# Optimization experiments

Measured on AMD Instinct MI355X. Metric: run time of the kernel, lower is better.

The kernel has to match this reference:

```python
import jax, jax.numpy as jnp
import numpy as np

N = 20000      # nodes
E = 160000     # edges (avg degree 8)
DIM_IN = 6     # node_dim_in (3 pos + 3 extra)
DIM = 3        # spatial dim used for edge vectors
L = 128        # node_dim_latent
A = 8          # atom_type_embed_dim
NL = 4         # nlayers
NMAX = 20      # nmax_atom_types
MAX_R = 50.0   # max_radius
EIN = 2 * L + 2 * A + 1  # message MLP input: y_src, y_dst, edge_attr(2A+1)


def smooth_cutoff(x):
    # e3nn-style smooth cutoff: 1 for x<0.5, cos ramp on [0.5,1], 0 beyond
    u = 2.0 * (x - 1.0)
    y = 0.5 * (1.0 - jnp.cos(jnp.pi * u))
    y = jnp.where(u > 0.0, 0.0, y)
    y = jnp.where(u < -1.0, 1.0, y)
    return y


def setup_inputs() -> dict:
    key = jax.random.key(0)
    ks = jax.random.split(key, 14)
    x = jax.random.normal(ks[0], (N, DIM_IN), dtype=jnp.float32) * 2.0
    batch = jnp.zeros((N,), dtype=jnp.int32)  # single graph; unused (con_fnc=None)
    node_attr = jax.random.randint(ks[1], (N, 1), 0, NMAX, dtype=jnp.int32)
    edge_src = jax.random.randint(ks[2], (E,), 0, N, dtype=jnp.int32)
    off = jax.random.randint(ks[3], (E,), 1, N, dtype=jnp.int32)
    edge_dst = (edge_src + off) % N  # no self-loops -> edge_len > 0
    # orthogonal uplift/project weight (torch parametrizations.orthogonal)
    W, _ = jnp.linalg.qr(jax.random.normal(ks[4], (L, DIM_IN), dtype=jnp.float32))  # [L, DIM_IN], orthonormal cols
    embed = jax.random.normal(ks[5], (NMAX, A), dtype=jnp.float32)
    h = jnp.ones((NL,), dtype=jnp.float32) * 0.01
    msg_w1 = jax.random.normal(ks[6], (NL, EIN, L), dtype=jnp.float32) / np.sqrt(EIN)
    msg_b1 = jnp.zeros((NL, L), dtype=jnp.float32)
    msg_w2 = jax.random.normal(ks[7], (NL, L, L), dtype=jnp.float32) / np.sqrt(L)
    msg_b2 = jnp.zeros((NL, L), dtype=jnp.float32)
    node_w1 = jax.random.normal(ks[8], (NL, 2 * L, L), dtype=jnp.float32) / np.sqrt(2 * L)
    node_b1 = jnp.zeros((NL, L), dtype=jnp.float32)
    node_w2 = jax.random.normal(ks[9], (NL, L, L), dtype=jnp.float32) / np.sqrt(L)
    node_b2 = jnp.zeros((NL, L), dtype=jnp.float32)
    return {"x": x, "batch": batch, "node_attr": node_attr, "edge_src": edge_src,
            "edge_dst": edge_dst, "W": W, "embed": embed, "h": h,
            "msg_w1": msg_w1, "msg_b1": msg_b1, "msg_w2": msg_w2, "msg_b2": msg_b2,
            "node_w1": node_w1, "node_b1": node_b1, "node_w2": node_w2, "node_b2": node_b2}


def _block(y, edge_attr, edge_src, edge_dst, w1, b1, w2, b2, nw1, nb1, nw2, nb2):
    # gather-compute-scatter message passing block
    m_in = jnp.concatenate([y[edge_src], y[edge_dst], edge_attr], axis=-1)  # [E, EIN]
    m = jax.nn.silu(m_in @ w1 + b1) @ w2 + b2                                # [E, L]
    agg = jax.ops.segment_sum(m, edge_dst, num_segments=N)                   # [N, L]
    u = jnp.concatenate([y, agg], axis=-1)                                   # [N, 2L]
    return jax.nn.silu(u @ nw1 + nb1) @ nw2 + nb2                            # [N, L]


def reference(x, batch, node_attr, edge_src, edge_dst, W, embed, h,
              msg_w1, msg_b1, msg_w2, msg_b2, node_w1, node_b1, node_w2, node_b2):
    attr_e = embed[jnp.min(node_attr, axis=-1)]  # [N, A]
    y = x @ W.T                                   # uplift [N, L]
    y_old = y
    for i in range(NL):
        pos = x[:, :DIM]
        edge_vec = pos[edge_src] - pos[edge_dst]
        edge_len = jnp.linalg.norm(edge_vec, axis=1)
        w = smooth_cutoff(edge_len / MAX_R) / edge_len
        edge_attr = jnp.concatenate([attr_e[edge_src], attr_e[edge_dst], w[:, None]], axis=-1)
        y_new = _block(y, edge_attr, edge_src, edge_dst,
                       msg_w1[i], msg_b1[i], msg_w2[i], msg_b2[i],
                       node_w1[i], node_b1[i], node_w2[i], node_b2[i])
        # leapfrog (gamma = 0)
        tmp = y
        y = 2.0 * y - y_old - (h[i] ** 2) * y_new
        y_old = tmp
        x = y @ W  # project back to low dim
    cv = jnp.float32(-1.0)
    reg = jnp.float32(0.0)
    return (x, cv, cv, reg, reg)
```

## Files before the change

### kernel.cpp

```cpp
#include <hip/hip_runtime.h>
#include <hip/hip_bf16.h>
#include <math.h>

#define N_ 20000
#define NPAD_ 20032
#define E_ 160000
#define DIM_IN_ 6
#define L_ 128
#define A_ 8
#define NL_ 4
#define EIN_ 273
#define MAX_R_ 50.0f

typedef unsigned short u16;
typedef short bf16x8 __attribute__((ext_vector_type(8)));
typedef u16   u16x8  __attribute__((ext_vector_type(8)));
typedef float f32x4  __attribute__((ext_vector_type(4)));

static __device__ __forceinline__ float bf2f(u16 u) {
    return __uint_as_float(((unsigned)u) << 16);
}
static __device__ __forceinline__ u16 f2bf(float f) {
    unsigned b = __float_as_uint(f);
    return (u16)((b + 0x7FFF + ((b >> 16) & 1)) >> 16);
}
static __device__ __forceinline__ float silu(float v) {
    return v / (1.f + __expf(-v));
}


__global__ void k_init_y(const float* __restrict__ x, const float* __restrict__ W,
                         float* __restrict__ y, float* __restrict__ y_old) {
    int tid = blockIdx.x * blockDim.x + threadIdx.x;
    if (tid >= N_ * L_) return;
    int n = tid >> 7, l = tid & 127;
    float a = 0.f;
#pragma unroll
    for (int d = 0; d < DIM_IN_; ++d) a = fmaf(x[n * DIM_IN_ + d], W[l * DIM_IN_ + d], a);
    y[tid] = a;
    y_old[tid] = a;
}

__global__ void k_attr(const int* __restrict__ node_attr, const float* __restrict__ embed,
                       float* __restrict__ attr_e) {
    int tid = blockIdx.x * blockDim.x + threadIdx.x;
    if (tid >= N_ * A_) return;
    int n = tid >> 3, a = tid & 7;
    attr_e[tid] = embed[node_attr[n] * A_ + a];
}

__global__ void k_pos(const float* __restrict__ y, const float* __restrict__ W,
                      const float* __restrict__ x_in, int layer,
                      float* __restrict__ pos4) {
    int tid = blockIdx.x * blockDim.x + threadIdx.x;
    if (tid >= N_ * 4) return;
    int n = tid >> 2, d = tid & 3;
    float v = 0.f;
    if (d < 3) {
        if (layer == 0) v = x_in[n * DIM_IN_ + d];
        else {
            for (int l = 0; l < L_; ++l) v = fmaf(y[(size_t)n * L_ + l], W[l * DIM_IN_ + d], v);
        }
    }
    pos4[tid] = v;
}

__global__ void k_x(const float* __restrict__ y, const float* __restrict__ W,
                    float* __restrict__ x_out) {
    int tid = blockIdx.x * blockDim.x + threadIdx.x;
    if (tid >= N_ * DIM_IN_) return;
    int n = tid / DIM_IN_, d = tid % DIM_IN_;
    float a = 0.f;
    for (int l = 0; l < L_; ++l) a = fmaf(y[(size_t)n * L_ + l], W[l * DIM_IN_ + d], a);
    x_out[tid] = a;
}

__global__ void k_scalars(float* __restrict__ tail) {
    int j = threadIdx.x;
    if (j < 4) tail[j] = (j < 2) ? -1.0f : 0.0f;
}


__global__ void k_hist(const int* __restrict__ edst, int* __restrict__ deg) {
    int e = blockIdx.x * blockDim.x + threadIdx.x;
    if (e < E_) atomicAdd(&deg[edst[e]], 1);
}

#define SCAN_CH 20
__global__ __launch_bounds__(1024) void k_scan(const int* __restrict__ deg,
                                               int* __restrict__ rowptr,
                                               int* __restrict__ cursor) {
    __shared__ int s[1024];
    int t = threadIdx.x;
    int base = t * SCAN_CH;
    int local[SCAN_CH];
    int sum = 0;
#pragma unroll
    for (int j = 0; j < SCAN_CH; ++j) {
        int n = base + j;
        int d = (n < N_) ? deg[n] : 0;
        local[j] = d; sum += d;
    }
    s[t] = sum;
    __syncthreads();
    for (int off = 1; off < 1024; off <<= 1) {
        int v = (t >= off) ? s[t - off] : 0;
        __syncthreads();
        s[t] += v;
        __syncthreads();
    }
    int run = t ? s[t - 1] : 0;
#pragma unroll
    for (int j = 0; j < SCAN_CH; ++j) {
        int n = base + j;
        if (n < N_) { rowptr[n] = run; cursor[n] = run; run += local[j]; }
    }
    if (t == 1023) rowptr[N_] = run;
}

__global__ void k_fill(const int* __restrict__ esrc, const int* __restrict__ edst,
                       int* __restrict__ cursor, int* __restrict__ csr_src) {
    int e = blockIdx.x * blockDim.x + threadIdx.x;
    if (e >= E_) return;
    int p = atomicAdd(&cursor[edst[e]], 1);
    csr_src[p] = esrc[e];
}

__global__ void k_prep(const float* __restrict__ mw1, const float* __restrict__ mb1,
                       const float* __restrict__ nw1, const float* __restrict__ nw2,
                       u16* __restrict__ w1cat_t, u16* __restrict__ nw1at,
                       u16* __restrict__ nw2t,
                       float* __restrict__ w1attr, float* __restrict__ bcat,
                       float* __restrict__ wr272) {
    int idx = blockIdx.x * 256 + threadIdx.x;
    if (idx < NL_ * 256 * 128) {
        int i = idx >> 15; int rem = idx & 32767; int cc = rem >> 7; int k = rem & 127;
        int row = (cc < 128) ? k : 128 + k;
        w1cat_t[idx] = f2bf(mw1[(size_t)i * EIN_ * L_ + row * L_ + (cc & 127)]);
        return;
    }
    idx -= NL_ * 256 * 128;
    if (idx < NL_ * 128 * 128) {
        int i = idx >> 14; int rem = idx & 16383; int c = rem >> 7; int k = rem & 127;
        nw1at[idx] = f2bf(nw1[(size_t)i * 2 * L_ * L_ + k * L_ + c]);
        return;
    }
    idx -= NL_ * 128 * 128;
    if (idx < NL_ * 128 * 128) {
        int i = idx >> 14; int rem = idx & 16383; int c = rem >> 7; int k = rem & 127;
        nw2t[idx] = f2bf(nw2[(size_t)i * L_ * L_ + k * L_ + c]);
        return;
    }
    idx -= NL_ * 128 * 128;
    if (idx < NL_ * 8 * 256) {
        int i = idx >> 11; int rem = idx & 2047; int j = rem >> 8; int cc = rem & 255;
        int row = (cc < 128) ? 256 + j : 264 + j;
        w1attr[idx] = mw1[(size_t)i * EIN_ * L_ + row * L_ + (cc & 127)];
        return;
    }
    idx -= NL_ * 8 * 256;
    if (idx < NL_ * 256) {
        int i = idx >> 8; int cc = idx & 255;
        bcat[idx] = (cc < 128) ? 0.f : mb1[i * L_ + cc - 128];
        return;
    }
    idx -= NL_ * 256;
    if (idx < NL_ * 128) {
        int i = idx >> 7; int c = idx & 127;
        wr272[idx] = mw1[(size_t)i * EIN_ * L_ + 272 * L_ + c];
    }
}
#define PREP_TOTAL (NL_*256*128 + 2*NL_*128*128 + NL_*8*256 + NL_*256 + NL_*128)

__global__ void k_prep2(const float* __restrict__ mw2, const float* __restrict__ mb2,
                        const float* __restrict__ nw1,
                        u16* __restrict__ W2nt, float* __restrict__ bvec) {
    int idx = blockIdx.x * 256 + threadIdx.x;
    if (idx < NL_ * 128 * 128) {
        int i = idx >> 14; int rem = idx & 16383; int c = rem >> 7; int k = rem & 127;
        const float* w2row = &mw2[(size_t)i * L_ * L_ + k * L_];
        const float* nb    = &nw1[(size_t)i * 2 * L_ * L_ + 128 * L_ + c];
        float a = 0.f;
        for (int j = 0; j < 128; ++j) a = fmaf(w2row[j], nb[(size_t)j * L_], a);
        W2nt[idx] = f2bf(a);
        return;
    }
    idx -= NL_ * 128 * 128;
    if (idx < NL_ * 128) {
        int i = idx >> 7; int c = idx & 127;
        const float* b2 = &mb2[i * L_];
        const float* nb = &nw1[(size_t)i * 2 * L_ * L_ + 128 * L_ + c];
        float a = 0.f;
        for (int j = 0; j < 128; ++j) a = fmaf(b2[j], nb[(size_t)j * L_], a);
        bvec[idx] = a;
    }
}
#define PREP2_TOTAL (NL_*128*128 + NL_*128)

__global__ __launch_bounds__(256) void k_pre(
    const float* __restrict__ y, const float* __restrict__ attr_e,
    const u16* __restrict__ w1cat_t,
    const float* __restrict__ w1attr,
    const float* __restrict__ bcat,
    u16* __restrict__ P) {
    __shared__ u16   s_a[64 * 136];
    __shared__ float s_attr[64 * 8];
    __shared__ float s_w1a[8 * 256];
    __shared__ float s_bc[256];

    const int t  = threadIdx.x;
    const int n0 = blockIdx.x * 64;

    for (int i = t; i < 64 * 16; i += 256) {
        int r = i >> 4, ch = i & 15;
        int n = n0 + r;
        u16x8 v;
        if (n < N_) {
            const float4* p = (const float4*)&y[(size_t)n * L_ + ch * 8];
            float4 f0 = p[0], f1 = p[1];
            v[0] = f2bf(f0.x); v[1] = f2bf(f0.y); v[2] = f2bf(f0.z); v[3] = f2bf(f0.w);
            v[4] = f2bf(f1.x); v[5] = f2bf(f1.y); v[6] = f2bf(f1.z); v[7] = f2bf(f1.w);
        } else {
#pragma unroll
            for (int j = 0; j < 8; ++j) v[j] = 0;
        }
        *(u16x8*)&s_a[r * 136 + ch * 8] = v;
    }
    for (int i = t; i < 64 * 2; i += 256) {
        int r = i >> 1, half = i & 1;
        int n = n0 + r;
        float4 v = make_float4(0.f, 0.f, 0.f, 0.f);
        if (n < N_) v = *(const float4*)&attr_e[(size_t)n * A_ + half * 4];
        *(float4*)&s_attr[r * 8 + half * 4] = v;
    }
    for (int i = t; i < 8 * 256; i += 256) s_w1a[i] = w1attr[i];
    if (t < 256) s_bc[t] = bcat[t];
    __syncthreads();

    const int l  = t & 63, w = t >> 6;
    const int r0 = w * 16;
    const int lr = l & 15, lk = l >> 4;

    bf16x8 a[4];
#pragma unroll
    for (int ks = 0; ks < 4; ++ks)
        a[ks] = *(const bf16x8*)&s_a[(r0 + lr) * 136 + ks * 32 + lk * 8];

#pragma unroll
    for (int cb = 0; cb < 2; ++cb) {
#pragma unroll
        for (int ct = 0; ct < 8; ++ct) {
            int cc = cb * 128 + ct * 16 + lr;
            float bb = s_bc[cc];
            f32x4 acc = {bb, bb, bb, bb};
#pragma unroll
            for (int ks = 0; ks < 4; ++ks) {
                bf16x8 b = *(const bf16x8*)&w1cat_t[(size_t)cc * 128 + ks * 32 + lk * 8];
                acc = __builtin_amdgcn_mfma_f32_16x16x32_bf16(a[ks], b, acc, 0, 0, 0);
            }
#pragma unroll
            for (int i = 0; i < 4; ++i) {
                int r = r0 + lk * 4 + i;
                int n = n0 + r;
                if (n < N_) {
                    float v = acc[i];
#pragma unroll
                    for (int j = 0; j < 8; ++j) v = fmaf(s_attr[r * 8 + j], s_w1a[j * 256 + cc], v);
                    P[(size_t)n * 256 + cc] = f2bf(v);
                }
            }
        }
    }
}

__global__ __launch_bounds__(256) void k_agg(
    const u16* __restrict__ P, const float* __restrict__ pos4,
    const int* __restrict__ csr_src, const int* __restrict__ rowptr,
    const float* __restrict__ wr272,
    u16* __restrict__ Hsum) {
    const int t = threadIdx.x;
    const int node = blockIdx.x * 4 + (t >> 6);
    const int l = t & 63;

    const int beg = rowptr[node], end = rowptr[node + 1];
    const float wr0 = wr272[2 * l], wr1 = wr272[2 * l + 1];
    unsigned pdu = *(const unsigned*)&P[(size_t)node * 256 + 128 + 2 * l];
    const float pd0 = bf2f((u16)pdu), pd1 = bf2f((u16)(pdu >> 16));
    const float4 pn = *(const float4*)&pos4[node * 4];

    float h0 = 0.f, h1 = 0.f;
    for (int cbeg = beg; cbeg < end; cbeg += 64) {
        const int cnt = min(64, end - cbeg);
        int   srcl = 0;
        float wl   = 0.f;
        if (l < cnt) {
            srcl = csr_src[cbeg + l];
            float4 ps = *(const float4*)&pos4[srcl * 4];
            float dx = ps.x - pn.x, dy = ps.y - pn.y, dz = ps.z - pn.z;
            float len = sqrtf(dx * dx + dy * dy + dz * dz);
            float u = 2.f * (len / MAX_R_ - 1.f);
            float cv;
            if (u > 0.f)       cv = 0.f;
            else if (u < -1.f) cv = 1.f;
            else               cv = 0.5f * (1.f - cosf(3.14159265358979323846f * u));
            wl = cv / len;
        }
        for (int i = 0; i < cnt; ++i) {
            int   s = __shfl(srcl, i, 64);
            float w = __shfl(wl,   i, 64);
            unsigned psu = *(const unsigned*)&P[(size_t)s * 256 + 2 * l];
            float v0 = bf2f((u16)psu)         + pd0 + w * wr0;
            float v1 = bf2f((u16)(psu >> 16)) + pd1 + w * wr1;
            h0 += silu(v0);
            h1 += silu(v1);
        }
    }
    unsigned out = (unsigned)f2bf(h0) | ((unsigned)f2bf(h1) << 16);
    *(unsigned*)&Hsum[(size_t)node * 128 + 2 * l] = out;
}

__global__ __launch_bounds__(256) void k_node(
    float* __restrict__ y, float* __restrict__ y_old,
    const u16* __restrict__ Hsum, const int* __restrict__ rowptr,
    const u16* __restrict__ nw1at,
    const u16* __restrict__ W2nt,
    const u16* __restrict__ nw2t,
    const float* __restrict__ bvec,
    const float* __restrict__ nb1,
    const float* __restrict__ nb2,
    const float* __restrict__ hvec, int layer) {
    __shared__ u16   s_a[64 * 136];
    __shared__ u16   s_h[64 * 136];
    __shared__ float s_deg[64];
    __shared__ float s_bv[128], s_b1[128], s_b2v[128];

    const int t  = threadIdx.x;
    const int n0 = blockIdx.x * 64;

    for (int i = t; i < 64 * 16; i += 256) {
        int r = i >> 4, ch = i & 15;
        int n = n0 + r;
        u16x8 v;
        if (n < N_) {
            const float4* p = (const float4*)&y[(size_t)n * L_ + ch * 8];
            float4 f0 = p[0], f1 = p[1];
            v[0] = f2bf(f0.x); v[1] = f2bf(f0.y); v[2] = f2bf(f0.z); v[3] = f2bf(f0.w);
            v[4] = f2bf(f1.x); v[5] = f2bf(f1.y); v[6] = f2bf(f1.z); v[7] = f2bf(f1.w);
        } else {
#pragma unroll
            for (int j = 0; j < 8; ++j) v[j] = 0;
        }
        *(u16x8*)&s_a[r * 136 + ch * 8] = v;
    }
    if (t < 128) { s_bv[t] = bvec[t]; s_b1[t] = nb1[t]; s_b2v[t] = nb2[t]; }
    else if (t < 192) {
        int r = t - 128, n = n0 + r;
        s_deg[r] = (n < N_) ? (float)(rowptr[n + 1] - rowptr[n]) : 0.f;
    }
    __syncthreads();

    const int l  = t & 63, w = t >> 6;
    const int r0 = w * 16;
    const int lr = l & 15, lk = l >> 4;

    bf16x8 ay[4], ah[4];
    const int nfr = n0 + r0 + lr;
#pragma unroll
    for (int ks = 0; ks < 4; ++ks) {
        ay[ks] = *(const bf16x8*)&s_a[(r0 + lr) * 136 + ks * 32 + lk * 8];
        ah[ks] = *(const bf16x8*)&Hsum[(size_t)nfr * 128 + ks * 32 + lk * 8];
    }

#pragma unroll
    for (int ct = 0; ct < 8; ++ct) {
        int c = ct * 16 + lr;
        f32x4 acc;
#pragma unroll
        for (int i = 0; i < 4; ++i)
            acc[i] = s_b1[c] + s_deg[r0 + lk * 4 + i] * s_bv[c];
#pragma unroll
        for (int ks = 0; ks < 4; ++ks) {
            bf16x8 b1f = *(const bf16x8*)&nw1at[(size_t)c * 128 + ks * 32 + lk * 8];
            acc = __builtin_amdgcn_mfma_f32_16x16x32_bf16(ay[ks], b1f, acc, 0, 0, 0);
        }
#pragma unroll
        for (int ks = 0; ks < 4; ++ks) {
            bf16x8 b2f = *(const bf16x8*)&W2nt[(size_t)c * 128 + ks * 32 + lk * 8];
            acc = __builtin_amdgcn_mfma_f32_16x16x32_bf16(ah[ks], b2f, acc, 0, 0, 0);
        }
#pragma unroll
        for (int i = 0; i < 4; ++i)
            s_h[(r0 + lk * 4 + i) * 136 + c] = f2bf(silu(acc[i]));
    }
    __syncthreads();

    bf16x8 a2[4];
#pragma unroll
    for (int ks = 0; ks < 4; ++ks)
        a2[ks] = *(const bf16x8*)&s_h[(r0 + lr) * 136 + ks * 32 + lk * 8];

    float hh = hvec[layer];
    float h2 = hh * hh;

#pragma unroll
    for (int ct = 0; ct < 8; ++ct) {
        int c = ct * 16 + lr;
        float bb = s_b2v[c];
        f32x4 acc = {bb, bb, bb, bb};
#pragma unroll
        for (int ks = 0; ks < 4; ++ks) {
            bf16x8 b = *(const bf16x8*)&nw2t[(size_t)c * 128 + ks * 32 + lk * 8];
            acc = __builtin_amdgcn_mfma_f32_16x16x32_bf16(a2[ks], b, acc, 0, 0, 0);
        }
#pragma unroll
        for (int i = 0; i < 4; ++i) {
            int n = n0 + r0 + lk * 4 + i;
            if (n < N_) {
                size_t idx = (size_t)n * L_ + c;
                float yv = y[idx], yo = y_old[idx];
                y_old[idx] = yv;
                y[idx] = 2.f * yv - yo - h2 * acc[i];
            }
        }
    }
}


#define ALLOC(ptr, T, count) T* ptr = (T*)base; base += (((size_t)(count) * sizeof(T)) + 255) / 256 * 256;

extern "C" void kernel_launch(void* const* d_in, const int* in_sizes, int n_in,
                              void* d_out, int out_size, void* d_ws, size_t ws_size,
                              hipStream_t stream) {
    const float* x_in      = (const float*)d_in[0];
    const int*   node_attr = (const int*)  d_in[2];
    const int*   esrc      = (const int*)  d_in[3];
    const int*   edst      = (const int*)  d_in[4];
    const float* W         = (const float*)d_in[5];
    const float* embed     = (const float*)d_in[6];
    const float* hvec      = (const float*)d_in[7];
    const float* mw1       = (const float*)d_in[8];
    const float* mb1       = (const float*)d_in[9];
    const float* mw2       = (const float*)d_in[10];
    const float* mb2       = (const float*)d_in[11];
    const float* nw1       = (const float*)d_in[12];
    const float* nb1       = (const float*)d_in[13];
    const float* nw2       = (const float*)d_in[14];
    const float* nb2       = (const float*)d_in[15];
    float* out = (float*)d_out;

    char* base = (char*)d_ws;
    ALLOC(y,       float, (size_t)N_ * L_);
    ALLOC(y_old,   float, (size_t)N_ * L_);
    ALLOC(attr_e,  float, (size_t)N_ * A_);
    ALLOC(pos4,    float, (size_t)N_ * 4);
    ALLOC(P,       u16,   (size_t)N_ * 256);
    ALLOC(Hsum,    u16,   (size_t)NPAD_ * 128);
    ALLOC(csr_src, int,   E_);
    ALLOC(deg,     int,   N_);
    ALLOC(rowptr,  int,   N_ + 1);
    ALLOC(cursor,  int,   N_);
    ALLOC(w1cat_t, u16,   (size_t)NL_ * 256 * 128);
    ALLOC(nw1at,   u16,   (size_t)NL_ * 128 * 128);
    ALLOC(nw2t,    u16,   (size_t)NL_ * 128 * 128);
    ALLOC(W2nt,    u16,   (size_t)NL_ * 128 * 128);
    ALLOC(w1attr,  float, (size_t)NL_ * 8 * 256);
    ALLOC(bcat,    float, (size_t)NL_ * 256);
    ALLOC(wr272,   float, (size_t)NL_ * 128);
    ALLOC(bvec,    float, (size_t)NL_ * 128);

    hipMemsetAsync(deg, 0, (size_t)N_ * sizeof(int), stream);
    k_prep<<<(PREP_TOTAL + 255) / 256, 256, 0, stream>>>(
        mw1, mb1, nw1, nw2, w1cat_t, nw1at, nw2t, w1attr, bcat, wr272);
    k_prep2<<<(PREP2_TOTAL + 255) / 256, 256, 0, stream>>>(mw2, mb2, nw1, W2nt, bvec);
    k_init_y<<<(N_ * L_ + 255) / 256, 256, 0, stream>>>(x_in, W, y, y_old);
    k_attr<<<(N_ * A_ + 255) / 256, 256, 0, stream>>>(node_attr, embed, attr_e);
    k_hist<<<(E_ + 255) / 256, 256, 0, stream>>>(edst, deg);
    k_scan<<<1, 1024, 0, stream>>>(deg, rowptr, cursor);
    k_fill<<<(E_ + 255) / 256, 256, 0, stream>>>(esrc, edst, cursor, csr_src);

    for (int i = 0; i < NL_; ++i) {
        k_pos<<<(N_ * 4 + 255) / 256, 256, 0, stream>>>(y, W, x_in, i, pos4);
        k_pre<<<313, 256, 0, stream>>>(
            y, attr_e,
            w1cat_t + (size_t)i * 256 * 128,
            w1attr + (size_t)i * 8 * 256,
            bcat + (size_t)i * 256,
            P);
        k_agg<<<N_ / 4, 256, 0, stream>>>(
            P, pos4, csr_src, rowptr,
            wr272 + (size_t)i * 128,
            Hsum);
        k_node<<<313, 256, 0, stream>>>(
            y, y_old, Hsum, rowptr,
            nw1at + (size_t)i * 128 * 128,
            W2nt + (size_t)i * 128 * 128,
            nw2t + (size_t)i * 128 * 128,
            bvec + (size_t)i * 128,
            nb1 + (size_t)i * L_,
            nb2 + (size_t)i * L_,
            hvec, i);
    }

    k_x<<<(N_ * DIM_IN_ + 255) / 256, 256, 0, stream>>>(y, W, out);
    k_scalars<<<1, 4, 0, stream>>>(out + (size_t)N_ * DIM_IN_);
}
```

Before: 495.8 us.

## Fuse next-layer position and message pre-projection into node update kernel

The per-layer k_pos and k_pre launches are removed. The node-update kernel now computes the next layer's projected positions and the first-layer message MLP pre-activation P directly from the freshly updated y, which it keeps in shared memory as bf16. Layer-0 positions move into k_init_y, and k_pre runs once before the loop. This drops two launches per layer and a reread of y. In exchange k_node uses more shared memory and registers, which may lower occupancy. Its pos computation also rereads y from global memory right after writing it.

```diff
diff --git a/kernel.cpp b/kernel.cpp
--- a/kernel.cpp
+++ b/kernel.cpp
@@ -30,8 +30,13 @@
 
 
 __global__ void k_init_y(const float* __restrict__ x, const float* __restrict__ W,
-                         float* __restrict__ y, float* __restrict__ y_old) {
+                         float* __restrict__ y, float* __restrict__ y_old,
+                         float* __restrict__ pos4) {
     int tid = blockIdx.x * blockDim.x + threadIdx.x;
+    if (tid < N_ * 4) {
+        int n = tid >> 2, d = tid & 3;
+        pos4[tid] = (d < 3) ? x[n * DIM_IN_ + d] : 0.f;
+    }
     if (tid >= N_ * L_) return;
     int n = tid >> 7, l = tid & 127;
     float a = 0.f;
@@ -47,22 +52,6 @@
     if (tid >= N_ * A_) return;
     int n = tid >> 3, a = tid & 7;
     attr_e[tid] = embed[node_attr[n] * A_ + a];
-}
-
-__global__ void k_pos(const float* __restrict__ y, const float* __restrict__ W,
-                      const float* __restrict__ x_in, int layer,
-                      float* __restrict__ pos4) {
-    int tid = blockIdx.x * blockDim.x + threadIdx.x;
-    if (tid >= N_ * 4) return;
-    int n = tid >> 2, d = tid & 3;
-    float v = 0.f;
-    if (d < 3) {
-        if (layer == 0) v = x_in[n * DIM_IN_ + d];
-        else {
-            for (int l = 0; l < L_; ++l) v = fmaf(y[(size_t)n * L_ + l], W[l * DIM_IN_ + d], v);
-        }
-    }
-    pos4[tid] = v;
 }
 
 __global__ void k_x(const float* __restrict__ y, const float* __restrict__ W,
@@ -328,11 +317,22 @@
     const float* __restrict__ bvec,
     const float* __restrict__ nb1,
     const float* __restrict__ nb2,
-    const float* __restrict__ hvec, int layer) {
+    const float* __restrict__ hvec, int layer,
+    int do_next,
+    const float* __restrict__ Wmat,
+    const float* __restrict__ attr_e,
+    const u16* __restrict__ w1cat_n,
+    const float* __restrict__ w1attr_n,
+    const float* __restrict__ bcat_n,
+    float* __restrict__ pos4, u16* __restrict__ P) {
     __shared__ u16   s_a[64 * 136];
     __shared__ u16   s_h[64 * 136];
     __shared__ float s_deg[64];
     __shared__ float s_bv[128], s_b1[128], s_b2v[128];
+    __shared__ float s_attr[64 * 8];
+    __shared__ float s_w1a[8 * 256];
+    __shared__ float s_bc[256];
+    __shared__ float s_W[128 * 3];
 
     const int t  = threadIdx.x;
     const int n0 = blockIdx.x * 64;
@@ -352,8 +352,21 @@
         }
         *(u16x8*)&s_a[r * 136 + ch * 8] = v;
     }
-    if (t < 128) { s_bv[t] = bvec[t]; s_b1[t] = nb1[t]; s_b2v[t] = nb2[t]; }
-    else if (t < 192) {
+    for (int i = t; i < 64 * 2; i += 256) {
+        int r = i >> 1, half = i & 1;
+        int n = n0 + r;
+        float4 v = make_float4(0.f, 0.f, 0.f, 0.f);
+        if (n < N_) v = *(const float4*)&attr_e[(size_t)n * A_ + half * 4];
+        *(float4*)&s_attr[r * 8 + half * 4] = v;
+    }
+    for (int i = t; i < 8 * 256; i += 256) s_w1a[i] = w1attr_n[i];
+    if (t < 256) s_bc[t] = bcat_n[t];
+    if (t < 128) {
+        s_bv[t] = bvec[t]; s_b1[t] = nb1[t]; s_b2v[t] = nb2[t];
+        s_W[t * 3 + 0] = Wmat[t * 6 + 0];
+        s_W[t * 3 + 1] = Wmat[t * 6 + 1];
+        s_W[t * 3 + 2] = Wmat[t * 6 + 2];
+    } else if (t < 192) {
         int r = t - 128, n = n0 + r;
         s_deg[r] = (n < N_) ? (float)(rowptr[n + 1] - rowptr[n]) : 0.f;
     }
@@ -414,12 +427,62 @@
         }
 #pragma unroll
         for (int i = 0; i < 4; ++i) {
-            int n = n0 + r0 + lk * 4 + i;
+            int r = r0 + lk * 4 + i;
+            int n = n0 + r;
+            float ny = 0.f;
             if (n < N_) {
                 size_t idx = (size_t)n * L_ + c;
                 float yv = y[idx], yo = y_old[idx];
                 y_old[idx] = yv;
-                y[idx] = 2.f * yv - yo - h2 * acc[i];
+                ny = 2.f * yv - yo - h2 * acc[i];
+                y[idx] = ny;
+            }
+            s_a[r * 136 + c] = f2bf(ny);
+        }
+    }
+
+    if (!do_next) return;
+    __syncthreads();
+
+    {
+        int r = t >> 2, d = t & 3;
+        int n = n0 + r;
+        if (n < N_) {
+            float v = 0.f;
+            if (d < 3)
+                for (int ll = 0; ll < L_; ++ll)
+                    v = fmaf(y[(size_t)n * L_ + ll], s_W[ll * 3 + d], v);
+            pos4[n * 4 + d] = v;
+        }
+    }
+
+    bf16x8 ap[4];
+#pragma unroll
+    for (int ks = 0; ks < 4; ++ks)
+        ap[ks] = *(const bf16x8*)&s_a[(r0 + lr) * 136 + ks * 32 + lk * 8];
+
+#pragma unroll
+    for (int cb = 0; cb < 2; ++cb) {
+#pragma unroll
+        for (int ct = 0; ct < 8; ++ct) {
+            int cc = cb * 128 + ct * 16 + lr;
+            float bb = s_bc[cc];
+            f32x4 acc = {bb, bb, bb, bb};
+#pragma unroll
+            for (int ks = 0; ks < 4; ++ks) {
+                bf16x8 b = *(const bf16x8*)&w1cat_n[(size_t)cc * 128 + ks * 32 + lk * 8];
+                acc = __builtin_amdgcn_mfma_f32_16x16x32_bf16(ap[ks], b, acc, 0, 0, 0);
+            }
+#pragma unroll
+            for (int i = 0; i < 4; ++i) {
+                int r = r0 + lk * 4 + i;
+                int n = n0 + r;
+                if (n < N_) {
+                    float v = acc[i];
+#pragma unroll
+                    for (int j = 0; j < 8; ++j) v = fmaf(s_attr[r * 8 + j], s_w1a[j * 256 + cc], v);
+                    P[(size_t)n * 256 + cc] = f2bf(v);
+                }
             }
         }
     }
@@ -472,20 +535,17 @@
     k_prep<<<(PREP_TOTAL + 255) / 256, 256, 0, stream>>>(
         mw1, mb1, nw1, nw2, w1cat_t, nw1at, nw2t, w1attr, bcat, wr272);
     k_prep2<<<(PREP2_TOTAL + 255) / 256, 256, 0, stream>>>(mw2, mb2, nw1, W2nt, bvec);
-    k_init_y<<<(N_ * L_ + 255) / 256, 256, 0, stream>>>(x_in, W, y, y_old);
+    k_init_y<<<(N_ * L_ + 255) / 256, 256, 0, stream>>>(x_in, W, y, y_old, pos4);
     k_attr<<<(N_ * A_ + 255) / 256, 256, 0, stream>>>(node_attr, embed, attr_e);
     k_hist<<<(E_ + 255) / 256, 256, 0, stream>>>(edst, deg);
     k_scan<<<1, 1024, 0, stream>>>(deg, rowptr, cursor);
     k_fill<<<(E_ + 255) / 256, 256, 0, stream>>>(esrc, edst, cursor, csr_src);
 
+    k_pre<<<313, 256, 0, stream>>>(
+        y, attr_e, w1cat_t, w1attr, bcat, P);
+
     for (int i = 0; i < NL_; ++i) {
-        k_pos<<<(N_ * 4 + 255) / 256, 256, 0, stream>>>(y, W, x_in, i, pos4);
-        k_pre<<<313, 256, 0, stream>>>(
-            y, attr_e,
-            w1cat_t + (size_t)i * 256 * 128,
-            w1attr + (size_t)i * 8 * 256,
-            bcat + (size_t)i * 256,
-            P);
+        int nx = (i < 3) ? i + 1 : 3;
         k_agg<<<N_ / 4, 256, 0, stream>>>(
             P, pos4, csr_src, rowptr,
             wr272 + (size_t)i * 128,
@@ -498,7 +558,13 @@
             bvec + (size_t)i * 128,
             nb1 + (size_t)i * L_,
             nb2 + (size_t)i * L_,
-            hvec, i);
+            hvec, i,
+            (i < 3) ? 1 : 0,
+            W, attr_e,
+            w1cat_t + (size_t)nx * 256 * 128,
+            w1attr + (size_t)nx * 8 * 256,
+            bcat + (size_t)nx * 256,
+            pos4, P);
     }
 
     k_x<<<(N_ * DIM_IN_ + 255) / 256, 256, 0, stream>>>(y, W, out);
```

New measurement: 469.6 us. -5.3%, faster.
